# Optimization experiments

Hardware: AMD Instinct MI355X
Metric: run time of the kernel (lower is better)

## Reference

```python
import jax, jax.numpy as jnp
import numpy as np

B, T, HID = 64, 2048, 512
H_CLS, D_OUT = 1024, 10


def setup_inputs() -> dict:
    key = jax.random.key(0)
    ks = jax.random.split(key, 9)
    std = 0.05
    return {
        "numerical": jax.random.normal(ks[0], (B, 16), dtype=jnp.float32),
        "embedding": jax.random.normal(ks[1], (B, T, HID), dtype=jnp.float32),
        "weight": jax.random.normal(ks[2], (HID, HID), dtype=jnp.float32) * std,
        "bias": jax.random.normal(ks[3], (1, HID), dtype=jnp.float32) * std,
        "context_weight": jax.random.normal(ks[4], (HID, 1), dtype=jnp.float32) * std,
        "W1": jax.random.normal(ks[5], (HID, H_CLS), dtype=jnp.float32) * 0.02,
        "b1": jnp.zeros((H_CLS,), dtype=jnp.float32),
        "W2": jax.random.normal(ks[6], (H_CLS, D_OUT), dtype=jnp.float32) * 0.02,
        "b2": jnp.zeros((D_OUT,), dtype=jnp.float32),
    }


def reference(numerical, embedding, weight, bias, context_weight, W1, b1, W2, b2):
    # matrix_mul(embedding.permute(1,0,2), weight, bias): per-timestep mm+bias+tanh
    # fused into one batched op. embedding: [B, T, HID]
    u = jnp.tanh(jnp.einsum('bth,hk->btk', embedding, weight) + bias)  # [B,T,HID]
    # matrix_mul(u, context_weight): mm + tanh, squeeze last dim -> [B,T]
    scores = jnp.tanh(jnp.einsum('bth,ho->bto', u, context_weight))[..., 0]  # [B,T]
    attn = jax.nn.softmax(scores, axis=1)  # softmax over time
    # element_wise_mul: weighted sum over time -> [B, HID]
    ctx = jnp.einsum('bth,bt->bh', embedding, attn)
    # classifier: Linear -> ReLU -> Linear -> Softmax(dim=1)
    h = jax.nn.relu(ctx @ W1 + b1)
    logits = h @ W2 + b2
    return jax.nn.softmax(logits, axis=1)
```

## Files before the change

kernel.cpp:

```cpp
#include <hip/hip_runtime.h>
#include <hip/hip_bf16.h>

typedef unsigned short u16;
typedef __attribute__((ext_vector_type(4))) float f32x4;
typedef __attribute__((ext_vector_type(8))) short bf16x8;
typedef __attribute__((ext_vector_type(8))) unsigned short u16x8;
typedef __attribute__((ext_vector_type(4))) unsigned short u16x4;

#define B_    64
#define T_    2048
#define HID_  512
#define HCLS_ 1024
#define DOUT_ 10
#define M_    (B_ * T_)

__device__ __forceinline__ unsigned f2bf2(float a, float b) {
#if __has_builtin(__builtin_amdgcn_cvt_pk_bf16_f32)
  auto r = __builtin_amdgcn_cvt_pk_bf16_f32(a, b);
  unsigned u;
  __builtin_memcpy(&u, &r, 4);
  return u;
#else
  unsigned ua = __float_as_uint(a) + 0x8000u;
  unsigned ub = __float_as_uint(b) + 0x8000u;
  return __builtin_amdgcn_perm(ub, ua, 0x07060302);
#endif
}

__device__ __forceinline__ float fast_tanh(float x) {
  float e = __expf(2.0f * x);
  return 1.0f - __fdividef(2.0f, e + 1.0f);
}

__global__ __launch_bounds__(256) void cvt_w_kernel(const float* __restrict__ W,
                                                    u16* __restrict__ Wt2) {
  const int pair = blockIdx.x * 4 + (threadIdx.x >> 6);
  const int l = threadIdx.x & 63;
  const int jt = pair >> 4, ks = pair & 15;
  const int n = jt * 16 + (l & 15);
  const int k0 = ks * 32 + (l >> 4) * 8;
  union { unsigned u[4]; u16x8 v; } r;
#pragma unroll
  for (int j = 0; j < 4; ++j)
    r.u[j] = f2bf2(W[(size_t)(k0 + 2 * j) * HID_ + n],
                   W[(size_t)(k0 + 2 * j + 1) * HID_ + n]);
  *(u16x8*)(Wt2 + (size_t)pair * 512 + l * 8) = r.v;
}

__global__ __launch_bounds__(512, 4) void gemm_fused_kernel(
    const float* __restrict__ E, const u16* __restrict__ Wt2,
    const float* __restrict__ bias, const float* __restrict__ cw,
    float* __restrict__ num, float* __restrict__ den) {
  __shared__ u16 lA[64 * 512];
  __shared__ float red[8 * 64];
  __shared__ float earr[64];

  const int tid = threadIdx.x;
  const int m0 = blockIdx.x * 64;
  const int b = blockIdx.x >> 5;
  const int w = tid >> 6, l = tid & 63;
  const int lm = l & 15, lg = l >> 4;

  const int arow = tid >> 3;
  const int akq = tid & 7;
  const float* aptr = E + (size_t)(m0 + arow) * HID_ + akq * 4;
  const int arx = arow & 7;
  u16* awbase = lA + arow * 512 + (akq & 1) * 4;

  const u16* bbase = Wt2 + (size_t)w * 32768 + (size_t)l * 8;

  f32x4 acc[4][4] = {};
  bf16x8 bvC[4], bvN[4];
  float4 aregO, aregN;

  aregO = *(const float4*)(aptr);
  {
    union { unsigned u[2]; u16x4 v; } r;
    r.u[0] = f2bf2(aregO.x, aregO.y);
    r.u[1] = f2bf2(aregO.z, aregO.w);
    *(u16x4*)(awbase + (((akq >> 1)) ^ arx) * 8) = r.v;
  }
  aregO = *(const float4*)(aptr + 32);
#pragma unroll
  for (int j = 0; j < 4; ++j)
    bvC[j] = *(const bf16x8*)(bbase + j * 8192);
  __asm__ __volatile__("s_waitcnt lgkmcnt(0)\n\ts_barrier" ::: "memory");

#pragma unroll
  for (int ks = 0; ks < 16; ++ks) {
    if (ks < 14) aregN = *(const float4*)(aptr + (ks + 2) * 32);
    if (ks < 15) {
#pragma unroll
      for (int j = 0; j < 4; ++j)
        bvN[j] = *(const bf16x8*)(bbase + j * 8192 + (ks + 1) * 512);
    }
    const u16* abase = lA + lm * 512 + (((ks * 4 + lg) ^ (lm & 7)) * 8);
#pragma unroll
    for (int i = 0; i < 4; ++i) {
      bf16x8 af = *(const bf16x8*)(abase + i * 16 * 512);
#pragma unroll
      for (int j = 0; j < 4; ++j)
        acc[i][j] = __builtin_amdgcn_mfma_f32_16x16x32_bf16(af, bvC[j], acc[i][j], 0, 0, 0);
    }
    if (ks < 15) {
      union { unsigned u[2]; u16x4 v; } r;
      r.u[0] = f2bf2(aregO.x, aregO.y);
      r.u[1] = f2bf2(aregO.z, aregO.w);
      *(u16x4*)(awbase + ((((ks + 1) * 4) + (akq >> 1)) ^ arx) * 8) = r.v;
    }
    aregO = aregN;
#pragma unroll
    for (int j = 0; j < 4; ++j) bvC[j] = bvN[j];
    __asm__ __volatile__("s_waitcnt lgkmcnt(0)\n\ts_barrier" ::: "memory");
  }

  __syncthreads();
  float bj[4], cj[4];
#pragma unroll
  for (int j = 0; j < 4; ++j) {
    int n = w * 64 + j * 16 + lm;
    bj[j] = bias[n];
    cj[j] = cw[n];
  }
#pragma unroll
  for (int i = 0; i < 4; ++i) {
#pragma unroll
    for (int r = 0; r < 4; ++r) {
      float s = 0.f;
#pragma unroll
      for (int j = 0; j < 4; ++j)
        s = fmaf(fast_tanh(acc[i][j][r] + bj[j]), cj[j], s);
      s += __shfl_xor(s, 1, 64);
      s += __shfl_xor(s, 2, 64);
      s += __shfl_xor(s, 4, 64);
      s += __shfl_xor(s, 8, 64);
      if (lm == 0) red[w * 64 + i * 16 + lg * 4 + r] = s;
    }
  }
  __syncthreads();
  if (tid < 64) {
    float d = 0.f;
#pragma unroll
    for (int ww = 0; ww < 8; ++ww) d += red[ww * 64 + tid];
    float e = __expf(fast_tanh(d));
    earr[tid] = e;
    float se = e;
    se += __shfl_xor(se, 1, 64);
    se += __shfl_xor(se, 2, 64);
    se += __shfl_xor(se, 4, 64);
    se += __shfl_xor(se, 8, 64);
    se += __shfl_xor(se, 16, 64);
    se += __shfl_xor(se, 32, 64);
    if (tid == 0) atomicAdd(den + b, se);
  }
  __syncthreads();
  {
    const int c8 = tid >> 3, rb = tid & 7;
    const u16* nbase = lA + rb * 512 + ((c8 ^ rb) * 8);
    float a8[8] = {};
#pragma unroll
    for (int k = 0; k < 8; ++k) {
      int r = rb + 8 * k;
      float e = earr[r];
      u16x8 v = *(const u16x8*)(nbase + k * 8 * 512);
#pragma unroll
      for (int j = 0; j < 8; ++j)
        a8[j] = fmaf(e, __uint_as_float((unsigned)v[j] << 16), a8[j]);
    }
#pragma unroll
    for (int j = 0; j < 8; ++j) {
      a8[j] += __shfl_xor(a8[j], 1, 64);
      a8[j] += __shfl_xor(a8[j], 2, 64);
      a8[j] += __shfl_xor(a8[j], 4, 64);
    }
    if (rb == 0) {
#pragma unroll
      for (int j = 0; j < 8; ++j)
        atomicAdd(num + (size_t)b * HID_ + c8 * 8 + j, a8[j]);
    }
  }
}

__global__ __launch_bounds__(1024) void classifier_kernel(
    const float* __restrict__ num, const float* __restrict__ den,
    const float* __restrict__ W1, const float* __restrict__ b1,
    const float* __restrict__ W2, const float* __restrict__ b2,
    float* __restrict__ out) {
  __shared__ float sc[HID_];
  __shared__ float hbuf[HCLS_];
  __shared__ float lgs[DOUT_];
  int b = blockIdx.x, tid = threadIdx.x;
  if (tid < HID_) sc[tid] = num[(size_t)b * HID_ + tid] / den[b];
  __syncthreads();
  float a = b1[tid];
#pragma unroll 8
  for (int k = 0; k < HID_; ++k) a = fmaf(sc[k], W1[(size_t)k * HCLS_ + tid], a);
  hbuf[tid] = fmaxf(a, 0.f);
  __syncthreads();
  if (tid < 160) {
    int j = tid >> 4, p = tid & 15;
    float acc2 = 0.f;
    for (int k = p; k < HCLS_; k += 16) acc2 = fmaf(hbuf[k], W2[(size_t)k * DOUT_ + j], acc2);
    acc2 += __shfl_xor(acc2, 1, 64);
    acc2 += __shfl_xor(acc2, 2, 64);
    acc2 += __shfl_xor(acc2, 4, 64);
    acc2 += __shfl_xor(acc2, 8, 64);
    if (p == 0) lgs[j] = acc2 + b2[j];
  }
  __syncthreads();
  if (tid == 0) {
    float mx = lgs[0];
#pragma unroll
    for (int j = 1; j < DOUT_; ++j) mx = fmaxf(mx, lgs[j]);
    float ex[DOUT_], s = 0.f;
#pragma unroll
    for (int j = 0; j < DOUT_; ++j) { ex[j] = __expf(lgs[j] - mx); s += ex[j]; }
    float inv = 1.f / s;
#pragma unroll
    for (int j = 0; j < DOUT_; ++j) out[b * DOUT_ + j] = ex[j] * inv;
  }
}

extern "C" void kernel_launch(void* const* d_in, const int* in_sizes, int n_in,
                              void* d_out, int out_size, void* d_ws, size_t ws_size,
                              hipStream_t stream) {
  (void)in_sizes; (void)n_in; (void)out_size; (void)ws_size;
  const float* E    = (const float*)d_in[1];
  const float* W    = (const float*)d_in[2];
  const float* bias = (const float*)d_in[3];
  const float* cw   = (const float*)d_in[4];
  const float* W1   = (const float*)d_in[5];
  const float* b1   = (const float*)d_in[6];
  const float* W2   = (const float*)d_in[7];
  const float* b2   = (const float*)d_in[8];
  float* out = (float*)d_out;

  u16*   Wt2 = (u16*)d_ws;
  float* num = (float*)((char*)d_ws + (512 << 10));
  float* den = (float*)((char*)d_ws + (512 << 10) + B_ * HID_ * sizeof(float));

  hipMemsetAsync(num, 0, (B_ * HID_ + B_) * sizeof(float), stream);
  cvt_w_kernel<<<128, 256, 0, stream>>>(W, Wt2);
  gemm_fused_kernel<<<M_ / 64, 512, 0, stream>>>(E, Wt2, bias, cw, num, den);
  classifier_kernel<<<B_, 1024, 0, stream>>>(num, den, W1, b1, W2, b2, out);
}
```

Before: 533.1 us.

## Preload full A tile into LDS up front and drop per-k-step barriers

Instead of streaming the fp32 embedding tile into LDS one k-slice per iteration with a barrier each step, the kernel now loads the whole 64x512 tile with fully coalesced float4 reads in two batches of 8, converts it to bf16, writes it swizzled into LDS, and synchronizes once. The MFMA k-loop then runs with no barriers, only prefetching weight fragments. This removes 16 block-wide barriers and gives many loads in flight, at the cost of no overlap between the global load phase and the MFMA compute within a block and higher register pressure for the 8 float4 buffers.

```diff
diff --git a/kernel.cpp b/kernel.cpp
--- a/kernel.cpp
+++ b/kernel.cpp
@@ -61,34 +61,37 @@
   const int w = tid >> 6, l = tid & 63;
   const int lm = l & 15, lg = l >> 4;
 
-  const int arow = tid >> 3;
-  const int akq = tid & 7;
-  const float* aptr = E + (size_t)(m0 + arow) * HID_ + akq * 4;
-  const int arx = arow & 7;
-  u16* awbase = lA + arow * 512 + (akq & 1) * 4;
+  const float* ag = E + (size_t)m0 * HID_ + tid * 4;
+#pragma unroll
+  for (int h = 0; h < 2; ++h) {
+    float4 r[8];
+#pragma unroll
+    for (int s = 0; s < 8; ++s)
+      r[s] = *(const float4*)(ag + (size_t)(h * 8 + s) * 2048);
+#pragma unroll
+    for (int s = 0; s < 8; ++s) {
+      const int ss = h * 8 + s;
+      const int row = ss * 4 + (tid >> 7);
+      const int c = (tid & 127) >> 1;
+      const int phys = c ^ (row & 7);
+      union { unsigned u[2]; u16x4 v; } t;
+      t.u[0] = f2bf2(r[s].x, r[s].y);
+      t.u[1] = f2bf2(r[s].z, r[s].w);
+      *(u16x4*)(lA + row * 512 + phys * 8 + (tid & 1) * 4) = t.v;
+    }
+    __builtin_amdgcn_sched_barrier(0);
+  }
 
   const u16* bbase = Wt2 + (size_t)w * 32768 + (size_t)l * 8;
+  bf16x8 bvC[4], bvN[4];
+#pragma unroll
+  for (int j = 0; j < 4; ++j) bvC[j] = *(const bf16x8*)(bbase + j * 8192);
+
+  __syncthreads();
 
   f32x4 acc[4][4] = {};
-  bf16x8 bvC[4], bvN[4];
-  float4 aregO, aregN;
-
-  aregO = *(const float4*)(aptr);
-  {
-    union { unsigned u[2]; u16x4 v; } r;
-    r.u[0] = f2bf2(aregO.x, aregO.y);
-    r.u[1] = f2bf2(aregO.z, aregO.w);
-    *(u16x4*)(awbase + (((akq >> 1)) ^ arx) * 8) = r.v;
-  }
-  aregO = *(const float4*)(aptr + 32);
-#pragma unroll
-  for (int j = 0; j < 4; ++j)
-    bvC[j] = *(const bf16x8*)(bbase + j * 8192);
-  __asm__ __volatile__("s_waitcnt lgkmcnt(0)\n\ts_barrier" ::: "memory");
-
 #pragma unroll
   for (int ks = 0; ks < 16; ++ks) {
-    if (ks < 14) aregN = *(const float4*)(aptr + (ks + 2) * 32);
     if (ks < 15) {
 #pragma unroll
       for (int j = 0; j < 4; ++j)
@@ -103,18 +106,11 @@
         acc[i][j] = __builtin_amdgcn_mfma_f32_16x16x32_bf16(af, bvC[j], acc[i][j], 0, 0, 0);
     }
     if (ks < 15) {
-      union { unsigned u[2]; u16x4 v; } r;
-      r.u[0] = f2bf2(aregO.x, aregO.y);
-      r.u[1] = f2bf2(aregO.z, aregO.w);
-      *(u16x4*)(awbase + ((((ks + 1) * 4) + (akq >> 1)) ^ arx) * 8) = r.v;
-    }
-    aregO = aregN;
-#pragma unroll
-    for (int j = 0; j < 4; ++j) bvC[j] = bvN[j];
-    __asm__ __volatile__("s_waitcnt lgkmcnt(0)\n\ts_barrier" ::: "memory");
-  }
-
-  __syncthreads();
+#pragma unroll
+      for (int j = 0; j < 4; ++j) bvC[j] = bvN[j];
+    }
+  }
+
   float bj[4], cj[4];
 #pragma unroll
   for (int j = 0; j < 4; ++j) {
```

New measurement: 511.9 us. -4.0%, faster.
